# Optimization experiments

Measured on AMD Instinct MI355X. Metric: run time of the kernel, lower is better.

Reference implementation:

```python
import jax, jax.numpy as jnp
import numpy as np

N_EMBED = 768
NUM_HEADS = 12
HEAD_DIM = N_EMBED // NUM_HEADS
B, L = 4, 2048


def setup_inputs() -> dict:
    key = jax.random.key(0)
    ks = jax.random.split(key, 11)
    s = 0.02
    return {
        "key": jax.random.normal(ks[0], (B, L, N_EMBED), jnp.float32),
        "query": jax.random.normal(ks[1], (B, L, N_EMBED), jnp.float32),
        "value": jax.random.normal(ks[2], (B, L, N_EMBED), jnp.float32),
        "Wk": jax.random.normal(ks[3], (N_EMBED, N_EMBED), jnp.float32) * s,
        "bk": jnp.zeros((N_EMBED,), jnp.float32),
        "Wq": jax.random.normal(ks[4], (N_EMBED, N_EMBED), jnp.float32) * s,
        "bq": jnp.zeros((N_EMBED,), jnp.float32),
        "Wv": jax.random.normal(ks[5], (N_EMBED, N_EMBED), jnp.float32) * s,
        "bv": jnp.zeros((N_EMBED,), jnp.float32),
        "Wfc": jax.random.normal(ks[6], (N_EMBED, N_EMBED), jnp.float32) * s,
        "bfc": jnp.zeros((N_EMBED,), jnp.float32),
    }


def reference(key, query, value, Wk, bk, Wq, bq, Wv, bv, Wfc, bfc):
    # Linear projections (torch Linear: x @ W.T + b)
    k = key @ Wk.T + bk      # [B, Lk, D]
    q = query @ Wq.T + bq    # [B, Lq, D]
    v = value @ Wv.T + bv    # [B, Lv, D]
    Bsz, Lq = q.shape[0], q.shape[1]
    k = k.reshape(Bsz, -1, NUM_HEADS, HEAD_DIM)
    q = q.reshape(Bsz, Lq, NUM_HEADS, HEAD_DIM)
    v = v.reshape(Bsz, -1, NUM_HEADS, HEAD_DIM)
    # Full [B, H, Lq, Lk] score tensor, scaled by sqrt(n_embed) (faithful to source)
    energies = jnp.einsum("nqhd,nkhd->nhqk", q, k)
    attn = jax.nn.softmax(energies / jnp.sqrt(jnp.float32(N_EMBED)), axis=3)
    out = jnp.einsum("nhql,nlhd->nqhd", attn, v).reshape(Bsz, Lq, N_EMBED)
    return out @ Wfc.T + bfc
```

## Files before the change

### kernel.cpp

```cpp
#include <hip/hip_runtime.h>
#include <hip/hip_bf16.h>
#include <math.h>

#define NEMB 768
#define NH   12
#define HD   64
#define BSZ  4
#define SEQ  2048
#define MTOT (BSZ * SEQ)

#define SCALE_LOG2E 0.0520587833f

typedef short bf16x8 __attribute__((ext_vector_type(8)));
typedef short short4v __attribute__((ext_vector_type(4)));
typedef float f32x4 __attribute__((ext_vector_type(4)));
typedef unsigned u32x4 __attribute__((ext_vector_type(4)));

__device__ __forceinline__ short f2bf(float f) {
  __bf16 h = (__bf16)f;
  return __builtin_bit_cast(short, h);
}

__device__ __forceinline__ void g2l16(const short* g, short* l) {
  __builtin_amdgcn_global_load_lds((const __attribute__((address_space(1))) unsigned*)g,
                                   (__attribute__((address_space(3))) unsigned*)l, 16, 0, 0);
}

__device__ __forceinline__ int swz(int x) { return (x ^ (x >> 3)) & 7; }

__global__ __launch_bounds__(256) void cvt_all(
    const float* __restrict__ i0, const float* __restrict__ i1, const float* __restrict__ i2,
    const float* __restrict__ i3, const float* __restrict__ i4, const float* __restrict__ i5,
    const float* __restrict__ i6,
    short* __restrict__ o0, short* __restrict__ o1, short* __restrict__ o2,
    short* __restrict__ o3, short* __restrict__ o4, short* __restrict__ o5,
    short* __restrict__ o6) {
  const int ACT4 = (MTOT * NEMB) / 4;
  const int WGT4 = (NEMB * NEMB) / 4;
  const float* in; short* out; int n4;
  switch (blockIdx.y) {
    case 0: in = i0; out = o0; n4 = ACT4; break;
    case 1: in = i1; out = o1; n4 = ACT4; break;
    case 2: in = i2; out = o2; n4 = ACT4; break;
    case 3: in = i3; out = o3; n4 = WGT4; break;
    case 4: in = i4; out = o4; n4 = WGT4; break;
    case 5: in = i5; out = o5; n4 = WGT4; break;
    default: in = i6; out = o6; n4 = WGT4; break;
  }
  int i = blockIdx.x * 256 + threadIdx.x;
  if (i >= n4) return;
  float4 f = reinterpret_cast<const float4*>(in)[i];
  short4v s; s[0] = f2bf(f.x); s[1] = f2bf(f.y); s[2] = f2bf(f.z); s[3] = f2bf(f.w);
  reinterpret_cast<short4v*>(out)[i] = s;
}

__global__ __launch_bounds__(256) void gemm_qkv(
    const short* __restrict__ A0, const short* __restrict__ A1, const short* __restrict__ A2,
    const short* __restrict__ W0, const short* __restrict__ W1, const short* __restrict__ W2,
    const float* __restrict__ b0, const float* __restrict__ b1, const float* __restrict__ b2,
    short* __restrict__ O0, short* __restrict__ O1, short* __restrict__ O2) {
  __shared__ __align__(16) short As[2][128 * 32];
  __shared__ __align__(16) short Bs[2][128 * 32];
  const short* A; const short* W; const float* bias; short* O; float scl;
  switch (blockIdx.z) {
    case 0:  A = A0; W = W0; bias = b0; O = O0; scl = SCALE_LOG2E; break;
    case 1:  A = A1; W = W1; bias = b1; O = O1; scl = 1.f; break;
    default: A = A2; W = W2; bias = b2; O = O2; scl = 1.f; break;
  }
  const int tid = threadIdx.x;
  const int lane = tid & 63, w = tid >> 6;
  const int wr = w >> 1, wc = w & 1;
  const int l15 = lane & 15, l4 = lane >> 4;
  const int m0 = blockIdx.x * 128, n0 = blockIdx.y * 128;

  f32x4 acc[4][4] = {};

#pragma unroll
  for (int i = 0; i < 2; ++i) {
    const int idx = tid + i * 256;
    const int row = idx >> 2, u = idx & 3;
    g2l16(A + (size_t)(m0 + row) * NEMB + u * 8, &As[0][idx * 8]);
    g2l16(W + (size_t)(n0 + row) * NEMB + u * 8, &Bs[0][idx * 8]);
  }
  __syncthreads();

  const int NT = NEMB / 32;
  for (int t = 0; t < NT; ++t) {
    const int cur = t & 1;
    if (t + 1 < NT) {
      const int k0 = (t + 1) * 32;
#pragma unroll
      for (int i = 0; i < 2; ++i) {
        const int idx = tid + i * 256;
        const int row = idx >> 2, u = idx & 3;
        g2l16(A + (size_t)(m0 + row) * NEMB + k0 + u * 8, &As[cur ^ 1][idx * 8]);
        g2l16(W + (size_t)(n0 + row) * NEMB + k0 + u * 8, &Bs[cur ^ 1][idx * 8]);
      }
    }
    bf16x8 af[4], bfr[4];
#pragma unroll
    for (int m = 0; m < 4; ++m)
      af[m] = *reinterpret_cast<const bf16x8*>(&As[cur][(wr * 64 + m * 16 + l15) * 32 + l4 * 8]);
#pragma unroll
    for (int n = 0; n < 4; ++n)
      bfr[n] = *reinterpret_cast<const bf16x8*>(&Bs[cur][(wc * 64 + n * 16 + l15) * 32 + l4 * 8]);
#pragma unroll
    for (int m = 0; m < 4; ++m)
#pragma unroll
      for (int n = 0; n < 4; ++n)
        acc[m][n] = __builtin_amdgcn_mfma_f32_16x16x32_bf16(af[m], bfr[n], acc[m][n], 0, 0, 0);
    __syncthreads();
  }

  float bj[4];
#pragma unroll
  for (int n = 0; n < 4; ++n) bj[n] = bias[n0 + wc * 64 + n * 16 + l15];
#pragma unroll
  for (int m = 0; m < 4; ++m)
#pragma unroll
    for (int n = 0; n < 4; ++n) {
      const int col = n0 + wc * 64 + n * 16 + l15;
#pragma unroll
      for (int r = 0; r < 4; ++r) {
        const int row = m0 + wr * 64 + m * 16 + l4 * 4 + r;
        O[(size_t)row * NEMB + col] = f2bf((acc[m][n][r] + bj[n]) * scl);
      }
    }
}

__global__ __launch_bounds__(256) void gemm_fc(
    const short* __restrict__ A, const short* __restrict__ W,
    const float* __restrict__ bias, float* __restrict__ C) {
  __shared__ __align__(16) short As[2][128 * 32];
  __shared__ __align__(16) short Bs[2][64 * 32];
  const int tid = threadIdx.x;
  const int lane = tid & 63, w = tid >> 6;
  const int l15 = lane & 15, l4 = lane >> 4;
  const int m0 = blockIdx.x * 128, n0 = blockIdx.y * 64;

  f32x4 acc[2][4] = {};

#pragma unroll
  for (int i = 0; i < 2; ++i) {
    const int idx = tid + i * 256;
    const int row = idx >> 2, u = idx & 3;
    g2l16(A + (size_t)(m0 + row) * NEMB + u * 8, &As[0][idx * 8]);
  }
  {
    const int row = tid >> 2, u = tid & 3;
    g2l16(W + (size_t)(n0 + row) * NEMB + u * 8, &Bs[0][tid * 8]);
  }
  __syncthreads();

  const int NT = NEMB / 32;
  for (int t = 0; t < NT; ++t) {
    const int cur = t & 1;
    if (t + 1 < NT) {
      const int k0 = (t + 1) * 32;
#pragma unroll
      for (int i = 0; i < 2; ++i) {
        const int idx = tid + i * 256;
        const int row = idx >> 2, u = idx & 3;
        g2l16(A + (size_t)(m0 + row) * NEMB + k0 + u * 8, &As[cur ^ 1][idx * 8]);
      }
      const int row = tid >> 2, u = tid & 3;
      g2l16(W + (size_t)(n0 + row) * NEMB + k0 + u * 8, &Bs[cur ^ 1][tid * 8]);
    }
    bf16x8 af[2], bfr[4];
#pragma unroll
    for (int m = 0; m < 2; ++m)
      af[m] = *reinterpret_cast<const bf16x8*>(&As[cur][(w * 32 + m * 16 + l15) * 32 + l4 * 8]);
#pragma unroll
    for (int n = 0; n < 4; ++n)
      bfr[n] = *reinterpret_cast<const bf16x8*>(&Bs[cur][(n * 16 + l15) * 32 + l4 * 8]);
#pragma unroll
    for (int m = 0; m < 2; ++m)
#pragma unroll
      for (int n = 0; n < 4; ++n)
        acc[m][n] = __builtin_amdgcn_mfma_f32_16x16x32_bf16(af[m], bfr[n], acc[m][n], 0, 0, 0);
    __syncthreads();
  }

  float bj[4];
#pragma unroll
  for (int n = 0; n < 4; ++n) bj[n] = bias[n0 + n * 16 + l15];
#pragma unroll
  for (int m = 0; m < 2; ++m)
#pragma unroll
    for (int n = 0; n < 4; ++n) {
      const int col = n0 + n * 16 + l15;
#pragma unroll
      for (int r = 0; r < 4; ++r) {
        const int row = m0 + w * 32 + m * 16 + l4 * 4 + r;
        C[(size_t)row * NEMB + col] = acc[m][n][r] + bj[n];
      }
    }
}

__global__ __launch_bounds__(512) void attn_mfma(const short* __restrict__ qp, const short* __restrict__ kp,
                                                 const short* __restrict__ vp, short* __restrict__ ao) {
  __shared__ __align__(16) short Ks[2][64 * 64];
  __shared__ __align__(16) short Vt[2][64 * 64];
  __shared__ __align__(16) short Ps[8][16 * 72];
  const int tid = threadIdx.x, lane = tid & 63, w = tid >> 6;
  const int l15 = lane & 15, l4 = lane >> 4;
  const int wg = blockIdx.x;
  const int nid = (wg & 7) * 96 + (wg >> 3);
  const int q0 = (nid & 15) * 128;
  const int bh = nid >> 4;
  const int b = bh / NH, h = bh - b * NH;
  const size_t abase = (size_t)b * SEQ * NEMB + h * HD;

  bf16x8 qf[2];
#pragma unroll
  for (int kb = 0; kb < 2; ++kb)
    qf[kb] = *reinterpret_cast<const bf16x8*>(
        &qp[abase + (size_t)(q0 + w * 16 + l15) * NEMB + kb * 32 + l4 * 8]);

  const bool kstager = (w < 4);
  const int st = tid & 255;
  const int vkv2 = st >> 3, vd8 = st & 7;
  const int vu = vkv2 >> 2, vsub = vkv2 & 3;
  const int pch = l15 >> 3, pcl = l15 & 7;

  if (kstager) {
#pragma unroll
    for (int i = 0; i < 2; ++i) {
      const int idx = st + i * 256;
      const int row = idx >> 3, u = idx & 7;
      g2l16(kp + abase + (size_t)row * NEMB + (u ^ swz(row)) * 8, &Ks[0][idx * 8]);
    }
  } else {
    const short* vr = vp + abase + (size_t)(vkv2 * 2) * NEMB + vd8 * 8;
    bf16x8 v0 = *reinterpret_cast<const bf16x8*>(vr);
    bf16x8 v1 = *reinterpret_cast<const bf16x8*>(vr + NEMB);
    u32x4 a0 = __builtin_bit_cast(u32x4, v0);
    u32x4 a1 = __builtin_bit_cast(u32x4, v1);
#pragma unroll
    for (int jj = 0; jj < 4; ++jj) {
      unsigned lo = __builtin_amdgcn_perm(a1[jj], a0[jj], 0x05040100u);
      unsigned hi = __builtin_amdgcn_perm(a1[jj], a0[jj], 0x07060302u);
      const int d0 = vd8 * 8 + jj * 2;
      *reinterpret_cast<unsigned*>(reinterpret_cast<char*>(Vt[0]) + d0 * 128 + (vu ^ swz(d0)) * 16 + vsub * 4) = lo;
      *reinterpret_cast<unsigned*>(reinterpret_cast<char*>(Vt[0]) + (d0 + 1) * 128 + (vu ^ swz(d0 + 1)) * 16 + vsub * 4) = hi;
    }
  }
  __syncthreads();

  f32x4 o[4] = {};
  float lacc[4] = {0.f, 0.f, 0.f, 0.f};

  for (int kt = 0; kt < SEQ / 64; ++kt) {
    const int cur = kt & 1, nxt = cur ^ 1;
    const bool more = (kt + 1) < SEQ / 64;

    bf16x8 v0, v1;
    if (kstager) {
      if (more) {
#pragma unroll
        for (int i = 0; i < 2; ++i) {
          const int idx = st + i * 256;
          const int row = idx >> 3, u = idx & 7;
          g2l16(kp + abase + (size_t)((kt + 1) * 64 + row) * NEMB + (u ^ swz(row)) * 8,
                &Ks[nxt][idx * 8]);
        }
      }
    } else if (more) {
      const short* vr = vp + abase + (size_t)((kt + 1) * 64 + vkv2 * 2) * NEMB + vd8 * 8;
      v0 = *reinterpret_cast<const bf16x8*>(vr);
      v1 = *reinterpret_cast<const bf16x8*>(vr + NEMB);
    }

    f32x4 sf[4];
#pragma unroll
    for (int nf = 0; nf < 4; ++nf) {
      f32x4 a = {0.f, 0.f, 0.f, 0.f};
#pragma unroll
      for (int kb = 0; kb < 2; ++kb) {
        const int row = nf * 16 + l15;
        const int u = kb * 4 + l4;
        bf16x8 kf = *reinterpret_cast<const bf16x8*>(
            reinterpret_cast<char*>(Ks[cur]) + row * 128 + (u ^ swz(row)) * 16);
        a = __builtin_amdgcn_mfma_f32_16x16x32_bf16(qf[kb], kf, a, 0, 0, 0);
      }
      sf[nf] = a;
    }

#pragma unroll
    for (int nf = 0; nf < 4; ++nf)
#pragma unroll
      for (int r = 0; r < 4; ++r) {
        const float p = exp2f(sf[nf][r]);
        lacc[r] += p;
        Ps[w][(l4 * 4 + r) * 72 + (((nf * 2 + pch) ^ l4) << 3) + pcl] = f2bf(p);
      }

    if (!kstager && more) {
      u32x4 a0 = __builtin_bit_cast(u32x4, v0);
      u32x4 a1 = __builtin_bit_cast(u32x4, v1);
#pragma unroll
      for (int jj = 0; jj < 4; ++jj) {
        unsigned lo = __builtin_amdgcn_perm(a1[jj], a0[jj], 0x05040100u);
        unsigned hi = __builtin_amdgcn_perm(a1[jj], a0[jj], 0x07060302u);
        const int d0 = vd8 * 8 + jj * 2;
        *reinterpret_cast<unsigned*>(reinterpret_cast<char*>(Vt[nxt]) + d0 * 128 + (vu ^ swz(d0)) * 16 + vsub * 4) = lo;
        *reinterpret_cast<unsigned*>(reinterpret_cast<char*>(Vt[nxt]) + (d0 + 1) * 128 + (vu ^ swz(d0 + 1)) * 16 + vsub * 4) = hi;
      }
    }

#pragma unroll
    for (int kb = 0; kb < 2; ++kb) {
      bf16x8 pf = *reinterpret_cast<const bf16x8*>(
          &Ps[w][l15 * 72 + (((kb * 4 + l4) ^ ((l15 >> 2) & 3)) << 3)]);
#pragma unroll
      for (int df = 0; df < 4; ++df) {
        const int d = df * 16 + l15;
        const int u = kb * 4 + l4;
        bf16x8 vf = *reinterpret_cast<const bf16x8*>(
            reinterpret_cast<char*>(Vt[cur]) + d * 128 + (u ^ swz(d)) * 16);
        o[df] = __builtin_amdgcn_mfma_f32_16x16x32_bf16(pf, vf, o[df], 0, 0, 0);
      }
    }
    __syncthreads();
  }

#pragma unroll
  for (int r = 0; r < 4; ++r)
#pragma unroll
    for (int off = 1; off < 16; off <<= 1)
      lacc[r] += __shfl_xor(lacc[r], off, 64);

  float inv[4];
#pragma unroll
  for (int r = 0; r < 4; ++r) inv[r] = 1.f / lacc[r];

#pragma unroll
  for (int df = 0; df < 4; ++df)
#pragma unroll
    for (int r = 0; r < 4; ++r) {
      const int row = q0 + w * 16 + l4 * 4 + r;
      ao[abase + (size_t)row * NEMB + df * 16 + l15] = f2bf(o[df][r] * inv[r]);
    }
}

extern "C" void kernel_launch(void* const* d_in, const int* in_sizes, int n_in,
                              void* d_out, int out_size, void* d_ws, size_t ws_size,
                              hipStream_t stream) {
  const float* key   = (const float*)d_in[0];
  const float* query = (const float*)d_in[1];
  const float* value = (const float*)d_in[2];
  const float* Wk    = (const float*)d_in[3];
  const float* bk    = (const float*)d_in[4];
  const float* Wq    = (const float*)d_in[5];
  const float* bq    = (const float*)d_in[6];
  const float* Wv    = (const float*)d_in[7];
  const float* bv    = (const float*)d_in[8];
  const float* Wfc   = (const float*)d_in[9];
  const float* bfc   = (const float*)d_in[10];

  const size_t P = (size_t)MTOT * NEMB;
  const size_t WSZ = (size_t)NEMB * NEMB;
  short* ws  = (short*)d_ws;
  short* qb  = ws;
  short* kb2 = qb + P;
  short* vb2 = kb2 + P;
  short* wq  = vb2 + P;
  short* wk  = wq + WSZ;
  short* wv  = wk + WSZ;
  short* wf  = wv + WSZ;
  short* qpp = wf + WSZ;
  short* kpp = qpp + P;
  short* vpp = kpp + P;
  short* aop = vpp + P;

  cvt_all<<<dim3(P / 4 / 256, 7), 256, 0, stream>>>(
      query, key, value, Wq, Wk, Wv, Wfc, qb, kb2, vb2, wq, wk, wv, wf);

  gemm_qkv<<<dim3(MTOT / 128, NEMB / 128, 3), 256, 0, stream>>>(
      qb, kb2, vb2, wq, wk, wv, bq, bk, bv, qpp, kpp, vpp);

  attn_mfma<<<dim3(16 * BSZ * NH), 512, 0, stream>>>(qpp, kpp, vpp, aop);

  gemm_fc<<<dim3(MTOT / 128, NEMB / 64), 256, 0, stream>>>(aop, wf, bfc, (float*)d_out);
}
```

Baseline: 310.7 us.

## Switch attention kernel to 32x32x16 MFMA with 4 waves of 32 query rows

Attention now runs 4 waves per block, each owning 32 query rows, and uses 32x32x16 bf16 MFMA instructions for both QK^T and PV. Every thread stages both K (async global-to-LDS) and V (transposed) instead of splitting waves into K and V stagers. The P tile layout and swizzle are changed to match the 32x32 fragment layout, and exp2 uses the hardware intrinsic. The aim is to reuse each loaded K/V fragment across more rows and cut LDS traffic per FLOP. In exchange each thread holds more accumulator registers, and the larger per-wave tiles may reduce occupancy.

```diff
diff --git a/kernel.cpp b/kernel.cpp
--- a/kernel.cpp
+++ b/kernel.cpp
@@ -14,6 +14,7 @@
 typedef short bf16x8 __attribute__((ext_vector_type(8)));
 typedef short short4v __attribute__((ext_vector_type(4)));
 typedef float f32x4 __attribute__((ext_vector_type(4)));
+typedef float f32x16 __attribute__((ext_vector_type(16)));
 typedef unsigned u32x4 __attribute__((ext_vector_type(4)));
 
 __device__ __forceinline__ short f2bf(float f) {
@@ -197,13 +198,13 @@
     }
 }
 
-__global__ __launch_bounds__(512) void attn_mfma(const short* __restrict__ qp, const short* __restrict__ kp,
-                                                 const short* __restrict__ vp, short* __restrict__ ao) {
+__global__ __launch_bounds__(256, 3) void attn_mfma(const short* __restrict__ qp, const short* __restrict__ kp,
+                                                    const short* __restrict__ vp, short* __restrict__ ao) {
   __shared__ __align__(16) short Ks[2][64 * 64];
   __shared__ __align__(16) short Vt[2][64 * 64];
-  __shared__ __align__(16) short Ps[8][16 * 72];
+  __shared__ __align__(16) short Ps[4][32 * 64];
   const int tid = threadIdx.x, lane = tid & 63, w = tid >> 6;
-  const int l15 = lane & 15, l4 = lane >> 4;
+  const int j = lane & 31, hi = lane >> 5;
   const int wg = blockIdx.x;
   const int nid = (wg & 7) * 96 + (wg >> 3);
   const int q0 = (nid & 15) * 128;
@@ -211,26 +212,23 @@
   const int b = bh / NH, h = bh - b * NH;
   const size_t abase = (size_t)b * SEQ * NEMB + h * HD;
 
-  bf16x8 qf[2];
-#pragma unroll
-  for (int kb = 0; kb < 2; ++kb)
-    qf[kb] = *reinterpret_cast<const bf16x8*>(
-        &qp[abase + (size_t)(q0 + w * 16 + l15) * NEMB + kb * 32 + l4 * 8]);
-
-  const bool kstager = (w < 4);
-  const int st = tid & 255;
-  const int vkv2 = st >> 3, vd8 = st & 7;
+  bf16x8 qf[4];
+#pragma unroll
+  for (int ks = 0; ks < 4; ++ks)
+    qf[ks] = *reinterpret_cast<const bf16x8*>(
+        &qp[abase + (size_t)(q0 + w * 32 + j) * NEMB + ks * 16 + hi * 8]);
+
+  const int vkv2 = tid >> 3, vd8 = tid & 7;
   const int vu = vkv2 >> 2, vsub = vkv2 & 3;
-  const int pch = l15 >> 3, pcl = l15 & 7;
-
-  if (kstager) {
-#pragma unroll
-    for (int i = 0; i < 2; ++i) {
-      const int idx = st + i * 256;
-      const int row = idx >> 3, u = idx & 7;
-      g2l16(kp + abase + (size_t)row * NEMB + (u ^ swz(row)) * 8, &Ks[0][idx * 8]);
-    }
-  } else {
+  const int swq = swz(j);
+
+#pragma unroll
+  for (int p = 0; p < 2; ++p) {
+    const int idx = tid + p * 256;
+    const int row = idx >> 3, u = idx & 7;
+    g2l16(kp + abase + (size_t)row * NEMB + (u ^ swz(row)) * 8, &Ks[0][idx * 8]);
+  }
+  {
     const short* vr = vp + abase + (size_t)(vkv2 * 2) * NEMB + vd8 * 8;
     bf16x8 v0 = *reinterpret_cast<const bf16x8*>(vr);
     bf16x8 v1 = *reinterpret_cast<const bf16x8*>(vr + NEMB);
@@ -239,107 +237,111 @@
 #pragma unroll
     for (int jj = 0; jj < 4; ++jj) {
       unsigned lo = __builtin_amdgcn_perm(a1[jj], a0[jj], 0x05040100u);
-      unsigned hi = __builtin_amdgcn_perm(a1[jj], a0[jj], 0x07060302u);
+      unsigned hi2 = __builtin_amdgcn_perm(a1[jj], a0[jj], 0x07060302u);
       const int d0 = vd8 * 8 + jj * 2;
       *reinterpret_cast<unsigned*>(reinterpret_cast<char*>(Vt[0]) + d0 * 128 + (vu ^ swz(d0)) * 16 + vsub * 4) = lo;
-      *reinterpret_cast<unsigned*>(reinterpret_cast<char*>(Vt[0]) + (d0 + 1) * 128 + (vu ^ swz(d0 + 1)) * 16 + vsub * 4) = hi;
+      *reinterpret_cast<unsigned*>(reinterpret_cast<char*>(Vt[0]) + (d0 + 1) * 128 + (vu ^ swz(d0 + 1)) * 16 + vsub * 4) = hi2;
     }
   }
   __syncthreads();
 
-  f32x4 o[4] = {};
-  float lacc[4] = {0.f, 0.f, 0.f, 0.f};
+  f32x16 o[2] = {};
+  float lacc[16];
+#pragma unroll
+  for (int r = 0; r < 16; ++r) lacc[r] = 0.f;
 
   for (int kt = 0; kt < SEQ / 64; ++kt) {
     const int cur = kt & 1, nxt = cur ^ 1;
     const bool more = (kt + 1) < SEQ / 64;
 
     bf16x8 v0, v1;
-    if (kstager) {
-      if (more) {
-#pragma unroll
-        for (int i = 0; i < 2; ++i) {
-          const int idx = st + i * 256;
-          const int row = idx >> 3, u = idx & 7;
-          g2l16(kp + abase + (size_t)((kt + 1) * 64 + row) * NEMB + (u ^ swz(row)) * 8,
-                &Ks[nxt][idx * 8]);
-        }
-      }
-    } else if (more) {
+    if (more) {
+#pragma unroll
+      for (int p = 0; p < 2; ++p) {
+        const int idx = tid + p * 256;
+        const int row = idx >> 3, u = idx & 7;
+        g2l16(kp + abase + (size_t)((kt + 1) * 64 + row) * NEMB + (u ^ swz(row)) * 8,
+              &Ks[nxt][idx * 8]);
+      }
       const short* vr = vp + abase + (size_t)((kt + 1) * 64 + vkv2 * 2) * NEMB + vd8 * 8;
       v0 = *reinterpret_cast<const bf16x8*>(vr);
       v1 = *reinterpret_cast<const bf16x8*>(vr + NEMB);
     }
 
-    f32x4 sf[4];
-#pragma unroll
-    for (int nf = 0; nf < 4; ++nf) {
-      f32x4 a = {0.f, 0.f, 0.f, 0.f};
-#pragma unroll
-      for (int kb = 0; kb < 2; ++kb) {
-        const int row = nf * 16 + l15;
-        const int u = kb * 4 + l4;
+    f32x16 sf[2];
+#pragma unroll
+    for (int cg = 0; cg < 2; ++cg) {
+      f32x16 a = {};
+      const int jk = cg * 32 + j;
+      const int sw = swz(jk);
+#pragma unroll
+      for (int ks = 0; ks < 4; ++ks) {
         bf16x8 kf = *reinterpret_cast<const bf16x8*>(
-            reinterpret_cast<char*>(Ks[cur]) + row * 128 + (u ^ swz(row)) * 16);
-        a = __builtin_amdgcn_mfma_f32_16x16x32_bf16(qf[kb], kf, a, 0, 0, 0);
-      }
-      sf[nf] = a;
-    }
-
-#pragma unroll
-    for (int nf = 0; nf < 4; ++nf)
-#pragma unroll
-      for (int r = 0; r < 4; ++r) {
-        const float p = exp2f(sf[nf][r]);
+            reinterpret_cast<char*>(Ks[cur]) + jk * 128 + (((ks << 1) + hi) ^ sw) * 16);
+        a = __builtin_amdgcn_mfma_f32_32x32x16_bf16(qf[ks], kf, a, 0, 0, 0);
+      }
+      sf[cg] = a;
+    }
+
+#pragma unroll
+    for (int cg = 0; cg < 2; ++cg) {
+      const int kvu = cg * 4 + (j >> 3);
+      const int kvl = j & 7;
+#pragma unroll
+      for (int r = 0; r < 16; ++r) {
+        const float p = __builtin_amdgcn_exp2f(sf[cg][r]);
         lacc[r] += p;
-        Ps[w][(l4 * 4 + r) * 72 + (((nf * 2 + pch) ^ l4) << 3) + pcl] = f2bf(p);
-      }
-
-    if (!kstager && more) {
+        const int qr = (r & 3) + 8 * (r >> 2) + 4 * hi;
+        Ps[w][qr * 64 + ((kvu ^ swz(qr)) << 3) + kvl] = f2bf(p);
+      }
+    }
+
+    if (more) {
       u32x4 a0 = __builtin_bit_cast(u32x4, v0);
       u32x4 a1 = __builtin_bit_cast(u32x4, v1);
 #pragma unroll
       for (int jj = 0; jj < 4; ++jj) {
         unsigned lo = __builtin_amdgcn_perm(a1[jj], a0[jj], 0x05040100u);
-        unsigned hi = __builtin_amdgcn_perm(a1[jj], a0[jj], 0x07060302u);
+        unsigned hi2 = __builtin_amdgcn_perm(a1[jj], a0[jj], 0x07060302u);
         const int d0 = vd8 * 8 + jj * 2;
         *reinterpret_cast<unsigned*>(reinterpret_cast<char*>(Vt[nxt]) + d0 * 128 + (vu ^ swz(d0)) * 16 + vsub * 4) = lo;
-        *reinterpret_cast<unsigned*>(reinterpret_cast<char*>(Vt[nxt]) + (d0 + 1) * 128 + (vu ^ swz(d0 + 1)) * 16 + vsub * 4) = hi;
-      }
-    }
-
-#pragma unroll
-    for (int kb = 0; kb < 2; ++kb) {
-      bf16x8 pf = *reinterpret_cast<const bf16x8*>(
-          &Ps[w][l15 * 72 + (((kb * 4 + l4) ^ ((l15 >> 2) & 3)) << 3)]);
-#pragma unroll
-      for (int df = 0; df < 4; ++df) {
-        const int d = df * 16 + l15;
-        const int u = kb * 4 + l4;
+        *reinterpret_cast<unsigned*>(reinterpret_cast<char*>(Vt[nxt]) + (d0 + 1) * 128 + (vu ^ swz(d0 + 1)) * 16 + vsub * 4) = hi2;
+      }
+    }
+
+    bf16x8 pa[4];
+#pragma unroll
+    for (int ks = 0; ks < 4; ++ks)
+      pa[ks] = *reinterpret_cast<const bf16x8*>(
+          &Ps[w][j * 64 + ((((ks << 1) + hi) ^ swq) << 3)]);
+#pragma unroll
+    for (int dg = 0; dg < 2; ++dg) {
+      const int jd = dg * 32 + j;
+      const int sw = swz(jd);
+#pragma unroll
+      for (int ks = 0; ks < 4; ++ks) {
         bf16x8 vf = *reinterpret_cast<const bf16x8*>(
-            reinterpret_cast<char*>(Vt[cur]) + d * 128 + (u ^ swz(d)) * 16);
-        o[df] = __builtin_amdgcn_mfma_f32_16x16x32_bf16(pf, vf, o[df], 0, 0, 0);
+            reinterpret_cast<char*>(Vt[cur]) + jd * 128 + (((ks << 1) + hi) ^ sw) * 16);
+        o[dg] = __builtin_amdgcn_mfma_f32_32x32x16_bf16(pa[ks], vf, o[dg], 0, 0, 0);
       }
     }
     __syncthreads();
   }
 
 #pragma unroll
-  for (int r = 0; r < 4; ++r)
-#pragma unroll
-    for (int off = 1; off < 16; off <<= 1)
+  for (int r = 0; r < 16; ++r) {
+#pragma unroll
+    for (int off = 1; off < 32; off <<= 1)
       lacc[r] += __shfl_xor(lacc[r], off, 64);
-
-  float inv[4];
-#pragma unroll
-  for (int r = 0; r < 4; ++r) inv[r] = 1.f / lacc[r];
-
-#pragma unroll
-  for (int df = 0; df < 4; ++df)
-#pragma unroll
-    for (int r = 0; r < 4; ++r) {
-      const int row = q0 + w * 16 + l4 * 4 + r;
-      ao[abase + (size_t)row * NEMB + df * 16 + l15] = f2bf(o[df][r] * inv[r]);
+    lacc[r] = 1.f / lacc[r];
+  }
+
+#pragma unroll
+  for (int dg = 0; dg < 2; ++dg)
+#pragma unroll
+    for (int r = 0; r < 16; ++r) {
+      const int row = q0 + w * 32 + (r & 3) + 8 * (r >> 2) + 4 * hi;
+      ao[abase + (size_t)row * NEMB + dg * 32 + j] = f2bf(o[dg][r] * lacc[r]);
     }
 }
 
@@ -379,7 +381,7 @@
   gemm_qkv<<<dim3(MTOT / 128, NEMB / 128, 3), 256, 0, stream>>>(
       qb, kb2, vb2, wq, wk, wv, bq, bk, bv, qpp, kpp, vpp);
 
-  attn_mfma<<<dim3(16 * BSZ * NH), 512, 0, stream>>>(qpp, kpp, vpp, aop);
+  attn_mfma<<<dim3(16 * BSZ * NH), 256, 0, stream>>>(qpp, kpp, vpp, aop);
 
   gemm_fc<<<dim3(MTOT / 128, NEMB / 64), 256, 0, stream>>>(aop, wf, bfc, (float*)d_out);
 }
```

Measured after the change: 285.4 us. 8.2% less time.
